# Kernel optimization log

Measured on AMD Instinct MI355X. Metric: run time of the kernel, lower is better.

## Reference

```python
import jax, jax.numpy as jnp
import numpy as np

EPS = 1e-5

def _causal_conv(x, w):
    # x: [B, Cin, S], w: [Cout, Cin, K]; left-pad by K-1 for causality
    k = w.shape[-1]
    x = jnp.pad(x, ((0, 0), (0, 0), (k - 1, 0)))
    return jax.lax.conv_general_dilated(x, w, (1,), 'VALID',
                                        dimension_numbers=('NCH', 'OIH', 'NCH'))

def _activate_norm(x):
    # relu -> mean-center over last axis -> scaled L2 normalize over last axis
    x = jax.nn.relu(x)
    x = x - x.mean(-1, keepdims=True)
    n = x.shape[-1]
    denom = (jnp.sqrt(jnp.sum(x * x, axis=-1, keepdims=True)) + EPS) * (n ** -0.5)
    return x / denom

def _feed_forward(x, w0, w1, w2):
    x = _causal_conv(x, w0)
    x = _activate_norm(x)
    x = _causal_conv(x, w1)
    x = _activate_norm(x)
    return _causal_conv(x, w2)

def setup_inputs() -> dict:
    key = jax.random.key(0)
    B, F, S = 4, 1024, 2048
    I, K = 2048, 5
    ks = jax.random.split(key, 12)
    def w(k, shape):
        fan_in = shape[1] * shape[2]
        return jax.random.normal(k, shape, jnp.float32) * (fan_in ** -0.5)
    inp = jax.random.normal(ks[0], (B, F, S), jnp.float32)
    pos_embd = jax.random.normal(ks[1], (1, F, S), jnp.float32) * 0.02
    divisor = jax.random.uniform(ks[2], (1, F, S), jnp.float32) + 0.5  # bounded away from 0
    return {
        'inp': inp, 'pos_embd': pos_embd, 'divisor': divisor,
        'dw0': w(ks[3], (I, F, 1)), 'dw1': w(ks[4], (I, I, K)), 'dw2': w(ks[5], (F, I, 1)),
        'sw0': w(ks[6], (I, F, 1)), 'sw1': w(ks[7], (I, I, K)), 'sw2': w(ks[8], (F, I, 1)),
        'hw0': w(ks[9], (I, F, 1)), 'hw1': w(ks[10], (I, I, K)), 'hw2': w(ks[11], (F, I, 1)),
    }

def reference(inp, pos_embd, divisor, dw0, dw1, dw2, sw0, sw1, sw2, hw0, hw1, hw2):
    out = inp + pos_embd
    depth = _feed_forward(out, dw0, dw1, dw2)
    scale = _feed_forward(out, sw0, sw1, sw2)
    shift = _feed_forward(out, hw0, hw1, hw2)
    # linear attention: cumsum over dim 1 (as in source), divide, scale/shift, norm, residual
    return inp + _activate_norm(jnp.cumsum(depth, axis=1) / divisor * scale + shift)
```

## Files before the change

kernel.cpp:

```cpp
#include <hip/hip_runtime.h>
#include <math.h>

#define BSZ 4
#define FCH 1024
#define SEQ 2048
#define ICH 2048
#define KW  5
#define EPSV 1e-5f
#define RPAD 2244
#define NCHF 16

typedef __attribute__((ext_vector_type(8))) short bf16x8;
typedef __attribute__((ext_vector_type(4))) float f32x4;
typedef __attribute__((ext_vector_type(4))) unsigned short us4;

__device__ __forceinline__ unsigned short f2bf(float f) {
  union { float f; unsigned u; } v; v.f = f;
  unsigned r = v.u + 0x7fff + ((v.u >> 16) & 1);
  return (unsigned short)(r >> 16);
}
__device__ __forceinline__ float bf2f(unsigned short u) {
  union { unsigned u; float f; } v; v.u = (unsigned)u << 16; return v.f;
}

__device__ __forceinline__ void gload_lds16(const void* g, void* l) {
  __builtin_amdgcn_global_load_lds(
      (const __attribute__((address_space(1))) void*)g,
      (__attribute__((address_space(3))) void*)l, 16, 0, 0);
}

__global__ __launch_bounds__(256) void addpos_T_kernel(
    const float* __restrict__ inp, const float* __restrict__ pos,
    unsigned short* __restrict__ X)
{
  __shared__ float t[64][65];
  const int s0 = blockIdx.x * 64, f0 = blockIdx.y * 64, b = blockIdx.z;
  const int a = threadIdx.x & 63, g = threadIdx.x >> 6;
  const float* ib = inp + (size_t)b * FCH * SEQ;
#pragma unroll
  for (int i = 0; i < 16; ++i) {
    const size_t o = (size_t)(f0 + g + i * 4) * SEQ + s0 + a;
    t[a][g + i * 4] = ib[o] + pos[o];
  }
  __syncthreads();
#pragma unroll
  for (int i = 0; i < 16; ++i)
    X[(size_t)b * RPAD * FCH + (size_t)(4 + s0 + g + i * 4) * FCH + f0 + a] =
        f2bf(t[g + i * 4][a]);
}

__global__ __launch_bounds__(256) void zero_xpad_kernel(unsigned short* __restrict__ X)
{
  const int i = blockIdx.x * 256 + threadIdx.x;
  const int b = i / (4 * FCH);
  const int r = i % (4 * FCH);
  X[(size_t)b * RPAD * FCH + r] = 0;
}

__global__ __launch_bounds__(256) void transpose_div_kernel(
    const float* __restrict__ D, float* __restrict__ O)
{
  __shared__ float t[64][65];
  const int s0 = blockIdx.x * 64, f0 = blockIdx.y * 64;
  const int a = threadIdx.x & 63, g = threadIdx.x >> 6;
#pragma unroll
  for (int i = 0; i < 16; ++i)
    t[a][g + i * 4] = D[(size_t)(f0 + g + i * 4) * SEQ + s0 + a];
  __syncthreads();
#pragma unroll
  for (int i = 0; i < 16; ++i)
    O[(size_t)(s0 + g + i * 4) * FCH + f0 + a] = t[g + i * 4][a];
}

__global__ __launch_bounds__(256) void cast_bf_kernel(
    const float* __restrict__ I, unsigned short* __restrict__ O)
{
  const size_t i = ((size_t)blockIdx.x * 256 + threadIdx.x) * 4;
  const float4 v = *(const float4*)(I + i);
  us4 o; o.x = f2bf(v.x); o.y = f2bf(v.y); o.z = f2bf(v.z); o.w = f2bf(v.w);
  *(us4*)(O + i) = o;
}

__global__ __launch_bounds__(256) void cast_w1_kernel(
    const float* __restrict__ W, unsigned short* __restrict__ O)
{
  const int c = blockIdx.x * 256 + threadIdx.x;
  const int m = blockIdx.y;
  const float* s = W + ((size_t)m * ICH + c) * KW;
#pragma unroll
  for (int k = 0; k < KW; ++k)
    O[((size_t)k * ICH + m) * ICH + c] = f2bf(s[k]);
}

template <int BN, int NTAPS, int OUTMODE>
__global__ __launch_bounds__(512, 2) void gemm256_kernel(
    const unsigned short* __restrict__ A, const unsigned short* __restrict__ W,
    void* __restrict__ Cv, int M, int K,
    float* __restrict__ P1, float* __restrict__ P2)
{
  extern __shared__ __align__(16) char lds[];
  constexpr int ABYTES = 32768;
  constexpr int BBYTES = BN * 128;
  constexpr int BUF = ABYTES + BBYTES;
  constexpr int WN  = BN / 4;
  constexpr int JF  = BN / 64;
  constexpr int JF2 = BN / 128;

  const int tid = threadIdx.x;
  const int ln  = tid & 63;
  const int wv  = tid >> 6;
  const int wr  = wv >> 2;
  const int wc  = wv & 3;
  const int l15 = ln & 15;
  const int lhi = ln >> 4;

  const int s0 = blockIdx.x * 256;
  const int m0 = blockIdx.y * BN;
  const int b  = blockIdx.z;

  const char* Ab = (const char*)(A + (size_t)b * RPAD * K);
  const char* Wb = (const char*)W;
  const size_t MK = (size_t)M * K;
  const int KT = K >> 6;

  const int scs  = (((tid & 7) ^ ((tid >> 3) & 7)) << 4);
  const int rxor = (l15 & 7) << 4;
  const int cbx0 = (lhi * 16) ^ rxor;
  const int cbx1 = (lhi * 16 + 64) ^ rxor;

  f32x4 acc[8][JF] = {};

  auto STAGE = [&](int t, int k0, int pb) {
    const int roff = (NTAPS == 1) ? 4 : t;
    char* dst = lds + pb * BUF;
#pragma unroll
    for (int q = 0; q < 4; ++q) {
      const int row = (q * 512 + tid) >> 3;
      gload_lds16(Ab + (size_t)(s0 + row + roff) * ((size_t)K * 2) +
                      (size_t)(k0 * 2 + scs),
                  dst + q * 8192 + tid * 16);
    }
#pragma unroll
    for (int q = 0; q < BN / 64; ++q) {
      const int row = (q * 512 + tid) >> 3;
      gload_lds16(Wb + ((size_t)t * MK + (size_t)(m0 + row) * K + k0) * 2 + scs,
                  dst + ABYTES + q * 8192 + tid * 16);
    }
  };

  auto COMPUTE = [&](int pb) {
    const char* bb = lds + pb * BUF;
    bf16x8 bw[2][JF2][2];
#pragma unroll
    for (int jh = 0; jh < 2; ++jh)
#pragma unroll
      for (int j = 0; j < JF2; ++j) {
        const int r = ABYTES + (wc * WN + jh * (WN / 2) + j * 16 + l15) * 128;
        bw[jh][j][0] = *(const bf16x8*)(bb + r + cbx0);
        bw[jh][j][1] = *(const bf16x8*)(bb + r + cbx1);
      }
#pragma unroll
    for (int ih = 0; ih < 2; ++ih) {
      bf16x8 af[4][2];
#pragma unroll
      for (int i = 0; i < 4; ++i) {
        const int r = (wr * 128 + ih * 64 + i * 16 + l15) * 128;
        af[i][0] = *(const bf16x8*)(bb + r + cbx0);
        af[i][1] = *(const bf16x8*)(bb + r + cbx1);
      }
#pragma unroll
      for (int jh = 0; jh < 2; ++jh) {
        __builtin_amdgcn_s_setprio(1);
#pragma unroll
        for (int i = 0; i < 4; ++i)
#pragma unroll
          for (int j = 0; j < JF2; ++j) {
            acc[ih * 4 + i][jh * JF2 + j] = __builtin_amdgcn_mfma_f32_16x16x32_bf16(
                af[i][0], bw[jh][j][0], acc[ih * 4 + i][jh * JF2 + j], 0, 0, 0);
            acc[ih * 4 + i][jh * JF2 + j] = __builtin_amdgcn_mfma_f32_16x16x32_bf16(
                af[i][1], bw[jh][j][1], acc[ih * 4 + i][jh * JF2 + j], 0, 0, 0);
          }
        __builtin_amdgcn_s_setprio(0);
      }
    }
  };

  STAGE(0, 0, 0);
  asm volatile("s_waitcnt vmcnt(0)" ::: "memory");
  __syncthreads();
  int p = 0;
  for (int t = 0; t < NTAPS; ++t) {
    for (int kt = 0; kt < KT; ++kt) {
      int ntp = t, nk = kt + 1;
      if (nk == KT) { nk = 0; ++ntp; }
      if (ntp < NTAPS) STAGE(ntp, nk * 64, p ^ 1);
      COMPUTE(p);
      asm volatile("s_waitcnt vmcnt(0)" ::: "memory");
      __syncthreads();
      p ^= 1;
    }
  }

  if constexpr (OUTMODE == 1) {
    unsigned short* Cb = (unsigned short*)Cv + (size_t)b * SEQ * M;
    float S[JF] = {}, Q[JF] = {};
#pragma unroll
    for (int i = 0; i < 8; ++i) {
      const int sb = s0 + wr * 128 + i * 16 + lhi * 4;
#pragma unroll
      for (int j = 0; j < JF; ++j) {
        const int m = m0 + wc * WN + j * 16 + l15;
#pragma unroll
        for (int r = 0; r < 4; ++r) {
          const float x = fmaxf(acc[i][j][r], 0.f);
          S[j] += x; Q[j] += x * x;
          Cb[(size_t)(sb + r) * M + m] = f2bf(x);
        }
      }
    }
#pragma unroll
    for (int j = 0; j < JF; ++j) {
      S[j] += __shfl_xor(S[j], 16, 64); S[j] += __shfl_xor(S[j], 32, 64);
      Q[j] += __shfl_xor(Q[j], 16, 64); Q[j] += __shfl_xor(Q[j], 32, 64);
    }
    float* SL = (float*)lds;
    float* QL = SL + 2 * 4 * JF * 16;
    if (lhi == 0) {
#pragma unroll
      for (int j = 0; j < JF; ++j) {
        SL[((wr * 4 + wc) * JF + j) * 16 + l15] = S[j];
        QL[((wr * 4 + wc) * JF + j) * 16 + l15] = Q[j];
      }
    }
    __syncthreads();
    if (wr == 0 && lhi == 0) {
#pragma unroll
      for (int j = 0; j < JF; ++j) {
        const int m = m0 + wc * WN + j * 16 + l15;
        const size_t o = ((size_t)b * (SEQ / 256) + blockIdx.x) * M + m;
        P1[o] = SL[((0 * 4 + wc) * JF + j) * 16 + l15] +
                SL[((1 * 4 + wc) * JF + j) * 16 + l15];
        P2[o] = QL[((0 * 4 + wc) * JF + j) * 16 + l15] +
                QL[((1 * 4 + wc) * JF + j) * 16 + l15];
      }
    }
  } else if constexpr (OUTMODE == 2) {
    unsigned short* Cb = (unsigned short*)Cv + (size_t)b * SEQ * M;
#pragma unroll
    for (int i = 0; i < 8; ++i) {
      const int sb = s0 + wr * 128 + i * 16 + lhi * 4;
#pragma unroll
      for (int j = 0; j < JF; ++j) {
        const int m = m0 + wc * WN + j * 16 + l15;
#pragma unroll
        for (int r = 0; r < 4; ++r)
          Cb[(size_t)(sb + r) * M + m] = f2bf(acc[i][j][r]);
      }
    }
  } else {
    float* Cb = (float*)Cv + (size_t)b * SEQ * M;
#pragma unroll
    for (int i = 0; i < 8; ++i) {
      const int sb = s0 + wr * 128 + i * 16 + lhi * 4;
#pragma unroll
      for (int j = 0; j < JF; ++j) {
        const int m = m0 + wc * WN + j * 16 + l15;
#pragma unroll
        for (int r = 0; r < 4; ++r)
          Cb[(size_t)(sb + r) * M + m] = acc[i][j][r];
      }
    }
  }
}

__global__ __launch_bounds__(256) void colred_kernel(
    const float* __restrict__ Cf, float* __restrict__ P1,
    float* __restrict__ P2, int M)
{
  const int b = blockIdx.z;
  const int mi = threadIdx.x & 63;
  const int sg = threadIdx.x >> 6;
  const int m = blockIdx.x * 64 + mi;
  const int s0 = blockIdx.y * 128;
  const float* src = Cf + ((size_t)b * SEQ + s0) * M + m;
  float sum = 0.f, sq = 0.f;
  for (int s = sg; s < 128; s += 4) {
    const float x = fmaxf(src[(size_t)s * M], 0.f);
    sum += x; sq += x * x;
  }
  __shared__ float rs[4][64], rq[4][64];
  rs[sg][mi] = sum; rq[sg][mi] = sq;
  __syncthreads();
  if (sg == 0) {
    const size_t o = ((size_t)b * NCHF + blockIdx.y) * M + m;
    P1[o] = rs[0][mi] + rs[1][mi] + rs[2][mi] + rs[3][mi];
    P2[o] = rq[0][mi] + rq[1][mi] + rq[2][mi] + rq[3][mi];
  }
}

__global__ __launch_bounds__(256) void colfin_kernel(
    const float* __restrict__ P1, const float* __restrict__ P2,
    float* __restrict__ MS, int M, int nchunk)
{
  const int i = blockIdx.x * 256 + threadIdx.x;
  const int b = i / M, m = i % M;
  float S1 = 0.f, S2 = 0.f;
  for (int c = 0; c < nchunk; ++c) {
    S1 += P1[((size_t)b * nchunk + c) * M + m];
    S2 += P2[((size_t)b * nchunk + c) * M + m];
  }
  const float mean = S1 * (1.f / SEQ);
  const float ss = fmaxf(S2 - SEQ * mean * mean, 0.f);
  const float scl = sqrtf((float)SEQ) / (sqrtf(ss) + EPSV);
  MS[((size_t)b * 2 + 0) * M + m] = mean;
  MS[((size_t)b * 2 + 1) * M + m] = scl;
}

__global__ __launch_bounds__(256) void colapply_kernel(
    const unsigned short* __restrict__ Cf, const float* __restrict__ MS,
    unsigned short* __restrict__ Ob, int M)
{
  const int b = blockIdx.z;
  const int mi = threadIdx.x & 63;
  const int sg = threadIdx.x >> 6;
  const int m = blockIdx.x * 64 + mi;
  const int s0 = blockIdx.y * 128;
  const float mean = MS[((size_t)b * 2 + 0) * M + m];
  const float scl  = MS[((size_t)b * 2 + 1) * M + m];
  const unsigned short* src = Cf + ((size_t)b * SEQ + s0) * M + m;
  unsigned short* dst = Ob + ((size_t)b * RPAD + 4 + s0) * M + m;
  if (blockIdx.y == 0 && sg == 0) {
#pragma unroll
    for (int r = 0; r < 4; ++r) Ob[((size_t)b * RPAD + r) * M + m] = 0;
  }
  for (int s = sg; s < 128; s += 4)
    dst[(size_t)s * M] = f2bf((bf2f(src[(size_t)s * M]) - mean) * scl);
}

__global__ __launch_bounds__(256) void combine_kernel(
    float* __restrict__ Dp, const float* __restrict__ divT,
    const unsigned short* __restrict__ Sc, const unsigned short* __restrict__ Sh)
{
  const int row = blockIdx.x * 4 + (threadIdx.x >> 6);
  const int b = row >> 11, s = row & 2047;
  const int ln = threadIdx.x & 63;
  const size_t base = ((size_t)b * SEQ + s) * FCH;
  const float* dv = divT + (size_t)s * FCH;
  float carry = 0.f;
  for (int c0 = 0; c0 < FCH; c0 += 64) {
    float x = Dp[base + c0 + ln];
#pragma unroll
    for (int d = 1; d < 64; d <<= 1) {
      const float t = __shfl_up(x, d, 64);
      if (ln >= d) x += t;
    }
    x += carry;
    carry = __shfl(x, 63, 64);
    Dp[base + c0 + ln] = x / dv[c0 + ln] * bf2f(Sc[base + c0 + ln]) +
                         bf2f(Sh[base + c0 + ln]);
  }
}

__global__ __launch_bounds__(256) void final_apply_kernel(
    const float* __restrict__ Df, const float* __restrict__ MS,
    const float* __restrict__ inp, float* __restrict__ out)
{
  __shared__ float tile[64][65];
  const int b = blockIdx.z;
  const int s0 = blockIdx.x * 64, f0 = blockIdx.y * 64;
  const int a = threadIdx.x & 63, g = threadIdx.x >> 6;
  const float mean = MS[((size_t)b * 2 + 0) * FCH + f0 + a];
  const float scl  = MS[((size_t)b * 2 + 1) * FCH + f0 + a];
#pragma unroll
  for (int i = 0; i < 16; ++i) {
    const int s = g + i * 4;
    const float x = fmaxf(Df[((size_t)b * SEQ + s0 + s) * FCH + f0 + a], 0.f);
    tile[s][a] = (x - mean) * scl;
  }
  __syncthreads();
#pragma unroll
  for (int i = 0; i < 16; ++i) {
    const int f = g + i * 4;
    const size_t o = ((size_t)b * FCH + f0 + f) * SEQ + s0 + a;
    out[o] = inp[o] + tile[a][f];
  }
}

extern "C" void kernel_launch(void* const* d_in, const int* in_sizes, int n_in,
                              void* d_out, int out_size, void* d_ws, size_t ws_size,
                              hipStream_t stream)
{
  const float* inp     = (const float*)d_in[0];
  const float* pos     = (const float*)d_in[1];
  const float* divisor = (const float*)d_in[2];
  const float* w_[9];
  for (int i = 0; i < 9; ++i) w_[i] = (const float*)d_in[3 + i];
  float* out = (float*)d_out;

  char* p = (char*)d_ws;
  float*          divT = (float*)p;          p += (size_t)SEQ * FCH * 4;
  unsigned short* Xbf  = (unsigned short*)p; p += (size_t)BSZ * RPAD * FCH * 2;
  unsigned short* T0b  = (unsigned short*)p; p += (size_t)BSZ * RPAD * ICH * 2;
  unsigned short* Cfb  = (unsigned short*)p; p += (size_t)BSZ * SEQ * ICH * 2;
  float*          Df   = (float*)p;          p += (size_t)BSZ * SEQ * FCH * 4;
  unsigned short* Sfb  = (unsigned short*)p; p += (size_t)BSZ * SEQ * FCH * 2;
  unsigned short* Hfb  = (unsigned short*)p; p += (size_t)BSZ * SEQ * FCH * 2;
  unsigned short* w0b  = (unsigned short*)p; p += (size_t)ICH * FCH * 2;
  unsigned short* w1b  = (unsigned short*)p; p += (size_t)KW * ICH * ICH * 2;
  unsigned short* w2b  = (unsigned short*)p; p += (size_t)FCH * ICH * 2;
  float*          P1   = (float*)p;          p += (size_t)BSZ * NCHF * ICH * 4;
  float*          P2   = (float*)p;          p += (size_t)BSZ * NCHF * ICH * 4;
  float*          MS   = (float*)p;          p += (size_t)BSZ * 2 * ICH * 4;

  hipFuncSetAttribute((const void*)gemm256_kernel<256, 1, 1>,
                      hipFuncAttributeMaxDynamicSharedMemorySize, 131072);
  hipFuncSetAttribute((const void*)gemm256_kernel<256, 5, 1>,
                      hipFuncAttributeMaxDynamicSharedMemorySize, 131072);
  hipFuncSetAttribute((const void*)gemm256_kernel<128, 1, 0>,
                      hipFuncAttributeMaxDynamicSharedMemorySize, 98304);
  hipFuncSetAttribute((const void*)gemm256_kernel<128, 1, 2>,
                      hipFuncAttributeMaxDynamicSharedMemorySize, 98304);

  zero_xpad_kernel<<<BSZ * 4 * FCH / 256, 256, 0, stream>>>(Xbf);
  addpos_T_kernel<<<dim3(SEQ / 64, FCH / 64, BSZ), 256, 0, stream>>>(inp, pos, Xbf);
  transpose_div_kernel<<<dim3(SEQ / 64, FCH / 64), 256, 0, stream>>>(divisor, divT);

  auto act_norm = [&](unsigned short* dst, int M) {
    colfin_kernel<<<(BSZ * M) / 256, 256, 0, stream>>>(P1, P2, MS, M, 8);
    colapply_kernel<<<dim3(M / 64, NCHF, BSZ), 256, 0, stream>>>(Cfb, MS, dst, M);
  };

  auto run_ff = [&](const float* w0, const float* w1, const float* w2,
                    void* dst, int mode2) {
    cast_bf_kernel<<<(ICH * FCH) / 1024, 256, 0, stream>>>(w0, w0b);
    cast_w1_kernel<<<dim3(ICH / 256, ICH), 256, 0, stream>>>(w1, w1b);
    cast_bf_kernel<<<(FCH * ICH) / 1024, 256, 0, stream>>>(w2, w2b);
    gemm256_kernel<256, 1, 1><<<dim3(SEQ / 256, ICH / 256, BSZ), 512, 131072, stream>>>(
        Xbf, w0b, Cfb, ICH, FCH, P1, P2);
    act_norm(T0b, ICH);
    gemm256_kernel<256, 5, 1><<<dim3(SEQ / 256, ICH / 256, BSZ), 512, 131072, stream>>>(
        T0b, w1b, Cfb, ICH, ICH, P1, P2);
    act_norm(T0b, ICH);
    if (mode2)
      gemm256_kernel<128, 1, 2><<<dim3(SEQ / 256, FCH / 128, BSZ), 512, 98304, stream>>>(
          T0b, w2b, dst, FCH, ICH, P1, P2);
    else
      gemm256_kernel<128, 1, 0><<<dim3(SEQ / 256, FCH / 128, BSZ), 512, 98304, stream>>>(
          T0b, w2b, dst, FCH, ICH, P1, P2);
  };

  run_ff(w_[0], w_[1], w_[2], Df, 0);
  run_ff(w_[3], w_[4], w_[5], Sfb, 1);
  run_ff(w_[6], w_[7], w_[8], Hfb, 1);

  combine_kernel<<<(BSZ * SEQ) / 4, 256, 0, stream>>>(Df, divT, Sfb, Hfb);

  colred_kernel<<<dim3(FCH / 64, NCHF, BSZ), 256, 0, stream>>>(Df, P1, P2, FCH);
  colfin_kernel<<<(BSZ * FCH) / 256, 256, 0, stream>>>(P1, P2, MS, FCH, NCHF);
  final_apply_kernel<<<dim3(SEQ / 64, FCH / 64, BSZ), 256, 0, stream>>>(
      Df, MS, inp, out);
}
```

Baseline: 1.189 ms.

## Use 4-stage LDS ring with K=32 tiles and counted vmcnt prefetch

The GEMM mainloop moves from a double-buffered K=64 tile with a full vmcnt(0) wait per step to a 4-slot ring of K=32 tiles. Loads are issued two steps ahead, and the loop waits with partial vmcnt counts before a raw s_barrier, so global loads stay in flight longer. The swizzle and fragment loads are adjusted for 64-byte rows, and a barrier is added before the epilogue reuses LDS. The trade-off is twice as many barriers per K, smaller MFMA batches per step, and a riskier hand-counted wait scheme.

New measurement: 1.390 ms. 1.17x slower.

```diff
diff --git a/kernel.cpp b/kernel.cpp
--- a/kernel.cpp
+++ b/kernel.cpp
@@ -29,6 +29,15 @@
       (__attribute__((address_space(3))) void*)l, 16, 0, 0);
 }
 
+template <int N> __device__ __forceinline__ void wait_vmcnt() {
+  if constexpr (N == 0) asm volatile("s_waitcnt vmcnt(0)" ::: "memory");
+  else if constexpr (N == 3) asm volatile("s_waitcnt vmcnt(3)" ::: "memory");
+  else if constexpr (N == 4) asm volatile("s_waitcnt vmcnt(4)" ::: "memory");
+}
+__device__ __forceinline__ void barrier_raw() {
+  asm volatile("s_barrier" ::: "memory");
+}
+
 __global__ __launch_bounds__(256) void addpos_T_kernel(
     const float* __restrict__ inp, const float* __restrict__ pos,
     unsigned short* __restrict__ X)
@@ -99,12 +108,12 @@
     float* __restrict__ P1, float* __restrict__ P2)
 {
   extern __shared__ __align__(16) char lds[];
-  constexpr int ABYTES = 32768;
-  constexpr int BBYTES = BN * 128;
+  constexpr int ABYTES = 16384;
+  constexpr int BBYTES = BN * 64;
   constexpr int BUF = ABYTES + BBYTES;
   constexpr int WN  = BN / 4;
   constexpr int JF  = BN / 64;
-  constexpr int JF2 = BN / 128;
+  constexpr int NL  = 2 + BN / 128;
 
   const int tid = threadIdx.x;
   const int ln  = tid & 63;
@@ -121,83 +130,70 @@
   const char* Ab = (const char*)(A + (size_t)b * RPAD * K);
   const char* Wb = (const char*)W;
   const size_t MK = (size_t)M * K;
-  const int KT = K >> 6;
-
-  const int scs  = (((tid & 7) ^ ((tid >> 3) & 7)) << 4);
-  const int rxor = (l15 & 7) << 4;
-  const int cbx0 = (lhi * 16) ^ rxor;
-  const int cbx1 = (lhi * 16 + 64) ^ rxor;
+  const size_t Kb2 = (size_t)K * 2;
+  const int KT = K >> 5;
+  const int T  = NTAPS * KT;
+
+  const int scs = (((tid & 3) ^ ((tid >> 2) & 3)) << 4);
+  const int row0 = tid >> 2;
 
   f32x4 acc[8][JF] = {};
 
-  auto STAGE = [&](int t, int k0, int pb) {
+  auto ISSUE = [&](int tau) {
+    const int t  = tau / KT;
+    const int k0 = (tau - t * KT) * 32;
     const int roff = (NTAPS == 1) ? 4 : t;
-    char* dst = lds + pb * BUF;
-#pragma unroll
-    for (int q = 0; q < 4; ++q) {
-      const int row = (q * 512 + tid) >> 3;
-      gload_lds16(Ab + (size_t)(s0 + row + roff) * ((size_t)K * 2) +
-                      (size_t)(k0 * 2 + scs),
+    char* dst = lds + (tau & 3) * BUF;
+#pragma unroll
+    for (int q = 0; q < 2; ++q) {
+      const int row = q * 128 + row0;
+      gload_lds16(Ab + (size_t)(s0 + row + roff) * Kb2 + (size_t)(k0 * 2 + scs),
                   dst + q * 8192 + tid * 16);
     }
 #pragma unroll
-    for (int q = 0; q < BN / 64; ++q) {
-      const int row = (q * 512 + tid) >> 3;
+    for (int q = 0; q < BN / 128; ++q) {
+      const int row = q * 128 + row0;
       gload_lds16(Wb + ((size_t)t * MK + (size_t)(m0 + row) * K + k0) * 2 + scs,
                   dst + ABYTES + q * 8192 + tid * 16);
     }
   };
 
-  auto COMPUTE = [&](int pb) {
-    const char* bb = lds + pb * BUF;
-    bf16x8 bw[2][JF2][2];
-#pragma unroll
-    for (int jh = 0; jh < 2; ++jh)
-#pragma unroll
-      for (int j = 0; j < JF2; ++j) {
-        const int r = ABYTES + (wc * WN + jh * (WN / 2) + j * 16 + l15) * 128;
-        bw[jh][j][0] = *(const bf16x8*)(bb + r + cbx0);
-        bw[jh][j][1] = *(const bf16x8*)(bb + r + cbx1);
-      }
-#pragma unroll
-    for (int ih = 0; ih < 2; ++ih) {
-      bf16x8 af[4][2];
-#pragma unroll
-      for (int i = 0; i < 4; ++i) {
-        const int r = (wr * 128 + ih * 64 + i * 16 + l15) * 128;
-        af[i][0] = *(const bf16x8*)(bb + r + cbx0);
-        af[i][1] = *(const bf16x8*)(bb + r + cbx1);
-      }
-#pragma unroll
-      for (int jh = 0; jh < 2; ++jh) {
-        __builtin_amdgcn_s_setprio(1);
-#pragma unroll
-        for (int i = 0; i < 4; ++i)
-#pragma unroll
-          for (int j = 0; j < JF2; ++j) {
-            acc[ih * 4 + i][jh * JF2 + j] = __builtin_amdgcn_mfma_f32_16x16x32_bf16(
-                af[i][0], bw[jh][j][0], acc[ih * 4 + i][jh * JF2 + j], 0, 0, 0);
-            acc[ih * 4 + i][jh * JF2 + j] = __builtin_amdgcn_mfma_f32_16x16x32_bf16(
-                af[i][1], bw[jh][j][1], acc[ih * 4 + i][jh * JF2 + j], 0, 0, 0);
-          }
-        __builtin_amdgcn_s_setprio(0);
-      }
-    }
+  auto COMPUTE = [&](int tau) {
+    const char* bb = lds + (tau & 3) * BUF;
+    bf16x8 bw[JF], af[8];
+#pragma unroll
+    for (int j = 0; j < JF; ++j) {
+      const int r = wc * WN + j * 16 + l15;
+      bw[j] = *(const bf16x8*)(bb + ABYTES + r * 64 +
+                               ((lhi * 16) ^ ((r & 3) << 4)));
+    }
+#pragma unroll
+    for (int i = 0; i < 8; ++i) {
+      const int r = wr * 128 + i * 16 + l15;
+      af[i] = *(const bf16x8*)(bb + r * 64 + ((lhi * 16) ^ ((r & 3) << 4)));
+    }
+    __builtin_amdgcn_s_setprio(1);
+#pragma unroll
+    for (int i = 0; i < 8; ++i)
+#pragma unroll
+      for (int j = 0; j < JF; ++j)
+        acc[i][j] = __builtin_amdgcn_mfma_f32_16x16x32_bf16(af[i], bw[j],
+                                                            acc[i][j], 0, 0, 0);
+    __builtin_amdgcn_s_setprio(0);
   };
 
-  STAGE(0, 0, 0);
-  asm volatile("s_waitcnt vmcnt(0)" ::: "memory");
-  __syncthreads();
-  int p = 0;
-  for (int t = 0; t < NTAPS; ++t) {
-    for (int kt = 0; kt < KT; ++kt) {
-      int ntp = t, nk = kt + 1;
-      if (nk == KT) { nk = 0; ++ntp; }
-      if (ntp < NTAPS) STAGE(ntp, nk * 64, p ^ 1);
-      COMPUTE(p);
-      asm volatile("s_waitcnt vmcnt(0)" ::: "memory");
-      __syncthreads();
-      p ^= 1;
+  ISSUE(0);
+  if (T > 1) { ISSUE(1); wait_vmcnt<NL>(); }
+  else       { wait_vmcnt<0>(); }
+  barrier_raw();
+
+  for (int tau = 0; tau < T; ++tau) {
+    if (tau + 2 < T) ISSUE(tau + 2);
+    COMPUTE(tau);
+    if (tau + 1 < T) {
+      if (tau + 2 < T) wait_vmcnt<NL>();
+      else             wait_vmcnt<0>();
+      barrier_raw();
     }
   }
 
@@ -225,6 +221,7 @@
     }
     float* SL = (float*)lds;
     float* QL = SL + 2 * 4 * JF * 16;
+    __syncthreads();
     if (lhi == 0) {
 #pragma unroll
       for (int j = 0; j < JF; ++j) {
```
